# Kernel tuning notes

Measured on AMD Instinct MI355X. Metric: run time of the kernel, lower is better.

The kernel has to match this reference:

```python
import jax, jax.numpy as jnp
import numpy as np

B, C, T = 128, 8, 128   # batch, channels, time steps
K, S = 20, 128          # known classes, barycenter length


def setup_inputs() -> dict:
    key = jax.random.key(0)
    k1, k2, k3, k4, k5 = jax.random.split(key, 5)
    x = jax.random.normal(k1, (B, C, T), dtype=jnp.float32)
    preds = jax.random.randint(k2, (B,), 0, K).astype(jnp.int32)
    barycenters = jax.random.normal(k3, (K, S, C), dtype=jnp.float32)
    # thresholds centered near realistic scales so both detector branches fire
    top_dist = 7.0 + 0.5 * jax.random.normal(k4, (K,), dtype=jnp.float32)
    bottom_cc = 25.0 + 5.0 * jax.random.normal(k5, (K, C), dtype=jnp.float32)
    return {"x": x, "preds": preds, "barycenters": barycenters,
            "top_dist": top_dist, "bottom_cc": bottom_cc}


def _dtw_dist(cost):
    """Classic DTW DP over a [T, S] sq-euclidean cost matrix; returns accumulated cost."""
    inf = jnp.asarray(jnp.inf, cost.dtype)
    row0 = jnp.cumsum(cost[0])  # first row: only left moves

    def row_step(prev, crow):
        prev_shift = jnp.concatenate([jnp.full((1,), inf, cost.dtype), prev[:-1]])
        def col_step(left, inp):
            c, p, ps = inp
            v = c + jnp.minimum(jnp.minimum(p, ps), left)
            return v, v
        _, row = jax.lax.scan(col_step, inf, (crow, prev, prev_shift))
        return row, None

    last, _ = jax.lax.scan(row_step, row0, cost[1:])
    return last[-1]


def reference(x, preds, barycenters, top_dist, bottom_cc):
    xt = jnp.transpose(x, (0, 2, 1))                    # [B, T, C]
    x2 = jnp.sum(xt * xt, axis=-1)                      # [B, T]
    b2 = jnp.sum(barycenters * barycenters, axis=-1)    # [K, S]
    dots = jnp.einsum('btc,ksc->bkts', xt, barycenters)  # [B, K, T, S]
    cost = jnp.maximum(x2[:, None, :, None] + b2[None, :, None, :] - 2.0 * dots, 0.0)

    Bn, Kn, Tn, Sn = cost.shape
    dists = jax.vmap(_dtw_dist)(cost.reshape(Bn * Kn, Tn, Sn)).reshape(Bn, Kn)
    log_dists = jnp.log(dists)
    dtw_unknown = jnp.all(log_dists > top_dist[None, :], axis=1)   # [B]

    # per-channel full cross-correlation max vs each barycenter
    corr_max = lambda a, v: jnp.max(jnp.correlate(a, v, mode='full'))
    per_ch = jax.vmap(corr_max, in_axes=(1, 1))          # over channels -> [C]
    per_cls = jax.vmap(per_ch, in_axes=(None, 0))        # over classes  -> [K, C]
    per_b = jax.vmap(per_cls, in_axes=(0, None))         # over batch    -> [B, K, C]
    ccs = per_b(xt, barycenters)
    # class 'fails' if any channel cc is not above its bottom threshold
    cc_unknown = jnp.all(jnp.any(ccs <= bottom_cc[None, :, :], axis=2), axis=1)  # [B]

    unknown = cc_unknown | dtw_unknown
    return jnp.where(unknown, Kn, preds)
```

## Files before the change

### kernel.cpp

```cpp
#include <hip/hip_runtime.h>
#include <hip/hip_bf16.h>
#include <math.h>

#define B_ 128
#define C_ 8
#define T_ 128
#define K_ 20
#define S_ 128

#define XROW 388
#define BTROW 132
#define SWZ(j) ((j) ^ ((((j) >> 5) & 7) << 2))
#define XP_GUARD 16
#define BT_BASE (4 * XROW + XP_GUARD)
#define SMEMF 3680

template <int CTRL, int RMASK>
__device__ __forceinline__ float dppf(float oldv, float v) {
    return __int_as_float(__builtin_amdgcn_update_dpp(
        __float_as_int(oldv), __float_as_int(v), CTRL, RMASK, 0xf, false));
}

__global__ __launch_bounds__(256) void fused_kernel(const float* __restrict__ x,
                                                    const float* __restrict__ bary,
                                                    const float* __restrict__ top_dist,
                                                    const float* __restrict__ bottom_cc,
                                                    int* __restrict__ dtw_gt,
                                                    int* __restrict__ cc_fail2) {
    __shared__ __align__(16) float smem[SMEMF];
    const float INF = __builtin_inff();
    int u = blockIdx.x;
    int tid = threadIdx.x;
    int w = tid >> 6;
    int lane = tid & 63;

    if (u % 3 == 0) {
        int pg = u / 3;
        int b  = pg / 5;
        int kg = pg - b * 5;
        int kk = kg * 4 + w;
        float* tile = smem;

        {
            int c  = tid >> 5;
            int t0 = (tid & 31) * 4;
            float4 v = *(const float4*)(x + ((size_t)b * C_ + c) * T_ + t0);
            tile[(t0 + 0) * 12 + c] = v.x;
            tile[(t0 + 1) * 12 + c] = v.y;
            tile[(t0 + 2) * 12 + c] = v.z;
            tile[(t0 + 3) * 12 + c] = v.w;
        }
        __syncthreads();
        if (tid < T_) {
            const float* rp = tile + tid * 12;
            float4 xa = *(const float4*)rp;
            float4 xh = *(const float4*)(rp + 4);
            float s = xa.x * xa.x;
            s = fmaf(xa.y, xa.y, s); s = fmaf(xa.z, xa.z, s); s = fmaf(xa.w, xa.w, s);
            s = fmaf(xh.x, xh.x, s); s = fmaf(xh.y, xh.y, s); s = fmaf(xh.z, xh.z, s);
            s = fmaf(xh.w, xh.w, s);
            tile[tid * 12 + 8] = s;
        }
        __syncthreads();

        float bv0[8], bv1[8], B20, B21;
        {
            const float4* bp = (const float4*)(bary + ((size_t)kk * S_ + 2 * lane) * C_);
            float4 q0 = bp[0], q1 = bp[1], q2 = bp[2], q3 = bp[3];
            bv0[0]=q0.x; bv0[1]=q0.y; bv0[2]=q0.z; bv0[3]=q0.w;
            bv0[4]=q1.x; bv0[5]=q1.y; bv0[6]=q1.z; bv0[7]=q1.w;
            bv1[0]=q2.x; bv1[1]=q2.y; bv1[2]=q2.z; bv1[3]=q2.w;
            bv1[4]=q3.x; bv1[5]=q3.y; bv1[6]=q3.z; bv1[7]=q3.w;
            float s0 = 0.f, s1 = 0.f;
            #pragma unroll
            for (int ch = 0; ch < 8; ++ch) {
                s0 = fmaf(bv0[ch], bv0[ch], s0);
                s1 = fmaf(bv1[ch], bv1[ch], s1);
            }
            B20 = s0; B21 = s1;
            #pragma unroll
            for (int ch = 0; ch < 8; ++ch) { bv0[ch] *= -2.f; bv1[ch] *= -2.f; }
        }

        float n0 = INF, n1 = INF;
        float dfix = (lane == 0) ? 0.f : INF;

        __builtin_amdgcn_s_setprio(1);
        float4 xa_n = *(const float4*)tile;
        float4 xh_n = *(const float4*)(tile + 4);
        float x2_n  = tile[8];

        #pragma unroll 2
        for (int t = 0; t < T_; ++t) {
            float4 xa = xa_n, xh = xh_n;
            float X2t = x2_n;
            const float* rpn = tile + ((t + 1) & (T_ - 1)) * 12;
            xa_n = *(const float4*)rpn;
            xh_n = *(const float4*)(rpn + 4);
            x2_n = rpn[8];

            float xv[8];
            xv[0]=xa.x; xv[1]=xa.y; xv[2]=xa.z; xv[3]=xa.w;
            xv[4]=xh.x; xv[5]=xh.y; xv[6]=xh.z; xv[7]=xh.w;
            float a0 = X2t + B20, a1 = X2t + B21;
            #pragma unroll
            for (int ch = 0; ch < 8; ++ch) {
                a0 = fmaf(bv0[ch], xv[ch], a0);
                a1 = fmaf(bv1[ch], xv[ch], a1);
            }
            a0 = fmaxf(a0, 0.f);
            a1 = fmaxf(a1, 0.f);

            float diag = dppf<0x138, 0xf>(INF, n1);
            float m0 = fminf(fminf(n0, diag), dfix);
            float m1 = fminf(n1, n0);
            dfix = INF;
            float C0 = a0 + m0;
            float C1 = a1 + m1;
            float C  = fminf(C1, C0 + a1);
            float A  = a0 + a1;

            float Ci, Ai;
            Ci = dppf<0x111, 0xf>(INF, C); Ai = dppf<0x111, 0xf>(0.f, A);
            C = fminf(C, Ci + A); A = A + Ai;
            Ci = dppf<0x112, 0xf>(INF, C); Ai = dppf<0x112, 0xf>(0.f, A);
            C = fminf(C, Ci + A); A = A + Ai;
            Ci = dppf<0x114, 0xf>(INF, C); Ai = dppf<0x114, 0xf>(0.f, A);
            C = fminf(C, Ci + A); A = A + Ai;
            Ci = dppf<0x118, 0xf>(INF, C); Ai = dppf<0x118, 0xf>(0.f, A);
            C = fminf(C, Ci + A); A = A + Ai;
            Ci = dppf<0x142, 0xa>(INF, C); Ai = dppf<0x142, 0xa>(0.f, A);
            C = fminf(C, Ci + A); A = A + Ai;
            Ci = dppf<0x143, 0xc>(INF, C); Ai = dppf<0x143, 0xc>(0.f, A);
            C = fminf(C, Ci + A); A = A + Ai;

            float Cp = dppf<0x138, 0xf>(INF, C);
            n0 = fminf(C0, Cp + a0);
            n1 = C;
        }
        __builtin_amdgcn_s_setprio(0);

        if (lane == 63)
            dtw_gt[b * K_ + kk] = (logf(n1) > top_dist[kk]) ? 1 : 0;
    } else {
        int cb = u - u / 3 - 1;
        int bh = cb / 5;
        int g5 = cb - bh * 5;
        int b  = bh >> 1;
        int h  = bh & 1;
        int kk = g5 * 4 + w;
        int cbase = h * 4;

        float* xp = smem;
        float* bt = smem + BT_BASE + w * (4 * BTROW);

        const float* xsrc = x + ((size_t)b * C_ + cbase) * T_;
        #pragma unroll
        for (int c = 0; c < 4; ++c) {
            for (int j = tid; j < XROW; j += 256) {
                int t = j - (S_ - 1);
                float v = (t >= 0 && t < T_) ? xsrc[c * T_ + t] : 0.f;
                xp[c * XROW + SWZ(j)] = v;
            }
        }
        #pragma unroll
        for (int r = 0; r < 2; ++r) {
            int s = r * 64 + lane;
            float4 q = *(const float4*)(bary + ((size_t)kk * S_ + s) * C_ + cbase);
            bt[0 * BTROW + s] = q.x;
            bt[1 * BTROW + s] = q.y;
            bt[2 * BTROW + s] = q.z;
            bt[3 * BTROW + s] = q.w;
        }
        __syncthreads();

        int cl = lane >> 4;
        int gl = lane & 15;
        int lag0 = gl << 4;
        const float* xr = xp + cl * XROW;
        const float* br = bt + cl * BTROW;

        float wdw[20];
        #pragma unroll
        for (int i = 0; i < 5; ++i) {
            float4 v = *(const float4*)&xr[SWZ(lag0 + i * 4)];
            wdw[i * 4 + 0] = v.x; wdw[i * 4 + 1] = v.y;
            wdw[i * 4 + 2] = v.z; wdw[i * 4 + 3] = v.w;
        }
        float acc[16];
        #pragma unroll
        for (int j = 0; j < 16; ++j) acc[j] = 0.f;

        #pragma unroll 8
        for (int s4 = 0; s4 < S_; s4 += 4) {
            float4 bq = *(const float4*)&br[s4];
            float bvals[4] = {bq.x, bq.y, bq.z, bq.w};
            #pragma unroll
            for (int uu = 0; uu < 4; ++uu) {
                #pragma unroll
                for (int j = 0; j < 16; ++j)
                    acc[j] = fmaf(wdw[uu + j], bvals[uu], acc[j]);
            }
            #pragma unroll
            for (int i = 0; i < 16; ++i) wdw[i] = wdw[i + 4];
            float4 v = *(const float4*)&xr[SWZ(lag0 + s4 + 20)];
            wdw[16] = v.x; wdw[17] = v.y; wdw[18] = v.z; wdw[19] = v.w;
        }

        if (gl == 15) acc[15] = -INF;
        float m = acc[0];
        #pragma unroll
        for (int j = 1; j < 16; ++j) m = fmaxf(m, acc[j]);
        #pragma unroll
        for (int off = 8; off >= 1; off >>= 1)
            m = fmaxf(m, __shfl_xor(m, off));

        bool fail = false;
        if (gl == 0) fail = (m <= bottom_cc[kk * C_ + cbase + cl]);
        unsigned long long bal = __ballot(fail);
        if (lane == 0) cc_fail2[(b * K_ + kk) * 2 + h] = (bal != 0ULL) ? 1 : 0;
    }
}

__global__ void final_kernel(const int* __restrict__ preds,
                             const int* __restrict__ dtw_gt,
                             const int* __restrict__ cc_fail2,
                             int* __restrict__ out) {
    int b = threadIdx.x;
    if (b < B_) {
        int dtw_all = 1, cc_all = 1;
        #pragma unroll
        for (int k = 0; k < K_; ++k) {
            dtw_all &= dtw_gt[b * K_ + k];
            cc_all &= (cc_fail2[(b * K_ + k) * 2] | cc_fail2[(b * K_ + k) * 2 + 1]);
        }
        out[b] = (dtw_all | cc_all) ? K_ : preds[b];
    }
}

extern "C" void kernel_launch(void* const* d_in, const int* in_sizes, int n_in,
                              void* d_out, int out_size, void* d_ws, size_t ws_size,
                              hipStream_t stream) {
    const float* x         = (const float*)d_in[0];
    const int*   preds     = (const int*)d_in[1];
    const float* bary      = (const float*)d_in[2];
    const float* top_dist  = (const float*)d_in[3];
    const float* bottom_cc = (const float*)d_in[4];
    int* out = (int*)d_out;

    int* dtw_gt   = (int*)d_ws;
    int* cc_fail2 = dtw_gt + B_ * K_;

    fused_kernel<<<1920, 256, 0, stream>>>(x, bary, top_dist, bottom_cc, dtw_gt, cc_fail2);
    final_kernel<<<1, 128, 0, stream>>>(preds, dtw_gt, cc_fail2, out);
}
```

Baseline: 72.43 us.

## Process two DTW class pairs per wave to interleave independent dependency chains

Each DTW wave now computes two (batch,class) DTW recurrences at once, so one block covers 8 pairs instead of 4. The DTW blocks are remapped to every fifth block, which lets a block span two batch rows, so two x tiles are loaded. The grid shrinks from 1920 to 1600 blocks. Interleaving the two independent DPP scan chains is meant to hide the latency of the serial cross-lane scan, at the cost of higher register pressure and fewer DTW waves running in parallel.

```diff
diff --git a/kernel.cpp b/kernel.cpp
--- a/kernel.cpp
+++ b/kernel.cpp
@@ -13,6 +13,7 @@
 #define SWZ(j) ((j) ^ ((((j) >> 5) & 7) << 2))
 #define XP_GUARD 16
 #define BT_BASE (4 * XROW + XP_GUARD)
+#define TILEF 1536
 #define SMEMF 3680
 
 template <int CTRL, int RMASK>
@@ -34,55 +35,78 @@
     int w = tid >> 6;
     int lane = tid & 63;
 
-    if (u % 3 == 0) {
-        int pg = u / 3;
-        int b  = pg / 5;
-        int kg = pg - b * 5;
-        int kk = kg * 4 + w;
-        float* tile = smem;
+    if (u % 5 == 0) {
+        int j  = u / 5;
+        int p0 = j * 8 + w * 2;
+        int b  = p0 / K_;
+        int k0 = p0 - b * K_;
+        int b_lo = (j * 8) / K_;
+        int b_hi = (j * 8 + 7) / K_;
+        float* tile0 = smem;
+        float* tile1 = smem + TILEF;
 
         {
             int c  = tid >> 5;
             int t0 = (tid & 31) * 4;
-            float4 v = *(const float4*)(x + ((size_t)b * C_ + c) * T_ + t0);
-            tile[(t0 + 0) * 12 + c] = v.x;
-            tile[(t0 + 1) * 12 + c] = v.y;
-            tile[(t0 + 2) * 12 + c] = v.z;
-            tile[(t0 + 3) * 12 + c] = v.w;
+            float4 v0 = *(const float4*)(x + ((size_t)b_lo * C_ + c) * T_ + t0);
+            float4 v1 = *(const float4*)(x + ((size_t)b_hi * C_ + c) * T_ + t0);
+            tile0[(t0 + 0) * 12 + c] = v0.x;
+            tile0[(t0 + 1) * 12 + c] = v0.y;
+            tile0[(t0 + 2) * 12 + c] = v0.z;
+            tile0[(t0 + 3) * 12 + c] = v0.w;
+            tile1[(t0 + 0) * 12 + c] = v1.x;
+            tile1[(t0 + 1) * 12 + c] = v1.y;
+            tile1[(t0 + 2) * 12 + c] = v1.z;
+            tile1[(t0 + 3) * 12 + c] = v1.w;
         }
         __syncthreads();
-        if (tid < T_) {
-            const float* rp = tile + tid * 12;
+        {
+            float* tt = (tid < T_) ? tile0 : tile1;
+            int t = tid & (T_ - 1);
+            const float* rp = tt + t * 12;
             float4 xa = *(const float4*)rp;
             float4 xh = *(const float4*)(rp + 4);
             float s = xa.x * xa.x;
             s = fmaf(xa.y, xa.y, s); s = fmaf(xa.z, xa.z, s); s = fmaf(xa.w, xa.w, s);
             s = fmaf(xh.x, xh.x, s); s = fmaf(xh.y, xh.y, s); s = fmaf(xh.z, xh.z, s);
             s = fmaf(xh.w, xh.w, s);
-            tile[tid * 12 + 8] = s;
+            tt[t * 12 + 8] = s;
         }
         __syncthreads();
 
-        float bv0[8], bv1[8], B20, B21;
+        const float* tile = (b == b_lo) ? tile0 : tile1;
+
+        float bvA0[8], bvA1[8], bvB0[8], bvB1[8], B2A0, B2A1, B2B0, B2B1;
         {
-            const float4* bp = (const float4*)(bary + ((size_t)kk * S_ + 2 * lane) * C_);
-            float4 q0 = bp[0], q1 = bp[1], q2 = bp[2], q3 = bp[3];
-            bv0[0]=q0.x; bv0[1]=q0.y; bv0[2]=q0.z; bv0[3]=q0.w;
-            bv0[4]=q1.x; bv0[5]=q1.y; bv0[6]=q1.z; bv0[7]=q1.w;
-            bv1[0]=q2.x; bv1[1]=q2.y; bv1[2]=q2.z; bv1[3]=q2.w;
-            bv1[4]=q3.x; bv1[5]=q3.y; bv1[6]=q3.z; bv1[7]=q3.w;
-            float s0 = 0.f, s1 = 0.f;
+            const float4* bpA = (const float4*)(bary + ((size_t)k0 * S_ + 2 * lane) * C_);
+            const float4* bpB = (const float4*)(bary + ((size_t)(k0 + 1) * S_ + 2 * lane) * C_);
+            float4 qa0 = bpA[0], qa1 = bpA[1], qa2 = bpA[2], qa3 = bpA[3];
+            float4 qb0 = bpB[0], qb1 = bpB[1], qb2 = bpB[2], qb3 = bpB[3];
+            bvA0[0]=qa0.x; bvA0[1]=qa0.y; bvA0[2]=qa0.z; bvA0[3]=qa0.w;
+            bvA0[4]=qa1.x; bvA0[5]=qa1.y; bvA0[6]=qa1.z; bvA0[7]=qa1.w;
+            bvA1[0]=qa2.x; bvA1[1]=qa2.y; bvA1[2]=qa2.z; bvA1[3]=qa2.w;
+            bvA1[4]=qa3.x; bvA1[5]=qa3.y; bvA1[6]=qa3.z; bvA1[7]=qa3.w;
+            bvB0[0]=qb0.x; bvB0[1]=qb0.y; bvB0[2]=qb0.z; bvB0[3]=qb0.w;
+            bvB0[4]=qb1.x; bvB0[5]=qb1.y; bvB0[6]=qb1.z; bvB0[7]=qb1.w;
+            bvB1[0]=qb2.x; bvB1[1]=qb2.y; bvB1[2]=qb2.z; bvB1[3]=qb2.w;
+            bvB1[4]=qb3.x; bvB1[5]=qb3.y; bvB1[6]=qb3.z; bvB1[7]=qb3.w;
+            float sA0=0.f, sA1=0.f, sB0=0.f, sB1=0.f;
             #pragma unroll
             for (int ch = 0; ch < 8; ++ch) {
-                s0 = fmaf(bv0[ch], bv0[ch], s0);
-                s1 = fmaf(bv1[ch], bv1[ch], s1);
-            }
-            B20 = s0; B21 = s1;
-            #pragma unroll
-            for (int ch = 0; ch < 8; ++ch) { bv0[ch] *= -2.f; bv1[ch] *= -2.f; }
-        }
-
-        float n0 = INF, n1 = INF;
+                sA0 = fmaf(bvA0[ch], bvA0[ch], sA0);
+                sA1 = fmaf(bvA1[ch], bvA1[ch], sA1);
+                sB0 = fmaf(bvB0[ch], bvB0[ch], sB0);
+                sB1 = fmaf(bvB1[ch], bvB1[ch], sB1);
+            }
+            B2A0 = sA0; B2A1 = sA1; B2B0 = sB0; B2B1 = sB1;
+            #pragma unroll
+            for (int ch = 0; ch < 8; ++ch) {
+                bvA0[ch] *= -2.f; bvA1[ch] *= -2.f;
+                bvB0[ch] *= -2.f; bvB1[ch] *= -2.f;
+            }
+        }
+
+        float nA0 = INF, nA1 = INF, nB0 = INF, nB1 = INF;
         float dfix = (lane == 0) ? 0.f : INF;
 
         __builtin_amdgcn_s_setprio(1);
@@ -102,48 +126,57 @@
             float xv[8];
             xv[0]=xa.x; xv[1]=xa.y; xv[2]=xa.z; xv[3]=xa.w;
             xv[4]=xh.x; xv[5]=xh.y; xv[6]=xh.z; xv[7]=xh.w;
-            float a0 = X2t + B20, a1 = X2t + B21;
+            float aA0 = X2t + B2A0, aA1 = X2t + B2A1;
+            float aB0 = X2t + B2B0, aB1 = X2t + B2B1;
             #pragma unroll
             for (int ch = 0; ch < 8; ++ch) {
-                a0 = fmaf(bv0[ch], xv[ch], a0);
-                a1 = fmaf(bv1[ch], xv[ch], a1);
-            }
-            a0 = fmaxf(a0, 0.f);
-            a1 = fmaxf(a1, 0.f);
-
-            float diag = dppf<0x138, 0xf>(INF, n1);
-            float m0 = fminf(fminf(n0, diag), dfix);
-            float m1 = fminf(n1, n0);
+                aA0 = fmaf(bvA0[ch], xv[ch], aA0);
+                aA1 = fmaf(bvA1[ch], xv[ch], aA1);
+                aB0 = fmaf(bvB0[ch], xv[ch], aB0);
+                aB1 = fmaf(bvB1[ch], xv[ch], aB1);
+            }
+            aA0 = fmaxf(aA0, 0.f); aA1 = fmaxf(aA1, 0.f);
+            aB0 = fmaxf(aB0, 0.f); aB1 = fmaxf(aB1, 0.f);
+
+            float diagA = dppf<0x138, 0xf>(INF, nA1);
+            float diagB = dppf<0x138, 0xf>(INF, nB1);
+            float mA0 = fminf(fminf(nA0, diagA), dfix);
+            float mB0 = fminf(fminf(nB0, diagB), dfix);
+            float mA1 = fminf(nA1, nA0);
+            float mB1 = fminf(nB1, nB0);
             dfix = INF;
-            float C0 = a0 + m0;
-            float C1 = a1 + m1;
-            float C  = fminf(C1, C0 + a1);
-            float A  = a0 + a1;
-
-            float Ci, Ai;
-            Ci = dppf<0x111, 0xf>(INF, C); Ai = dppf<0x111, 0xf>(0.f, A);
-            C = fminf(C, Ci + A); A = A + Ai;
-            Ci = dppf<0x112, 0xf>(INF, C); Ai = dppf<0x112, 0xf>(0.f, A);
-            C = fminf(C, Ci + A); A = A + Ai;
-            Ci = dppf<0x114, 0xf>(INF, C); Ai = dppf<0x114, 0xf>(0.f, A);
-            C = fminf(C, Ci + A); A = A + Ai;
-            Ci = dppf<0x118, 0xf>(INF, C); Ai = dppf<0x118, 0xf>(0.f, A);
-            C = fminf(C, Ci + A); A = A + Ai;
-            Ci = dppf<0x142, 0xa>(INF, C); Ai = dppf<0x142, 0xa>(0.f, A);
-            C = fminf(C, Ci + A); A = A + Ai;
-            Ci = dppf<0x143, 0xc>(INF, C); Ai = dppf<0x143, 0xc>(0.f, A);
-            C = fminf(C, Ci + A); A = A + Ai;
-
-            float Cp = dppf<0x138, 0xf>(INF, C);
-            n0 = fminf(C0, Cp + a0);
-            n1 = C;
+            float CA0 = aA0 + mA0, CA1 = aA1 + mA1;
+            float CB0 = aB0 + mB0, CB1 = aB1 + mB1;
+            float CA = fminf(CA1, CA0 + aA1);  float AA = aA0 + aA1;
+            float CB = fminf(CB1, CB0 + aB1);  float AB = aB0 + aB1;
+
+            float CiA, AiA, CiB, AiB;
+            #define SCAN_STEP(CTRL, RMASK)                                          \
+                CiA = dppf<CTRL, RMASK>(INF, CA); AiA = dppf<CTRL, RMASK>(0.f, AA); \
+                CiB = dppf<CTRL, RMASK>(INF, CB); AiB = dppf<CTRL, RMASK>(0.f, AB); \
+                CA = fminf(CA, CiA + AA); AA = AA + AiA;                            \
+                CB = fminf(CB, CiB + AB); AB = AB + AiB;
+            SCAN_STEP(0x111, 0xf)
+            SCAN_STEP(0x112, 0xf)
+            SCAN_STEP(0x114, 0xf)
+            SCAN_STEP(0x118, 0xf)
+            SCAN_STEP(0x142, 0xa)
+            SCAN_STEP(0x143, 0xc)
+            #undef SCAN_STEP
+
+            float CpA = dppf<0x138, 0xf>(INF, CA);
+            float CpB = dppf<0x138, 0xf>(INF, CB);
+            nA0 = fminf(CA0, CpA + aA0);  nA1 = CA;
+            nB0 = fminf(CB0, CpB + aB0);  nB1 = CB;
         }
         __builtin_amdgcn_s_setprio(0);
 
-        if (lane == 63)
-            dtw_gt[b * K_ + kk] = (logf(n1) > top_dist[kk]) ? 1 : 0;
+        if (lane == 63) {
+            dtw_gt[p0]     = (logf(nA1) > top_dist[k0])     ? 1 : 0;
+            dtw_gt[p0 + 1] = (logf(nB1) > top_dist[k0 + 1]) ? 1 : 0;
+        }
     } else {
-        int cb = u - u / 3 - 1;
+        int cb = u - u / 5 - 1;
         int bh = cb / 5;
         int g5 = cb - bh * 5;
         int b  = bh >> 1;
@@ -157,10 +190,10 @@
         const float* xsrc = x + ((size_t)b * C_ + cbase) * T_;
         #pragma unroll
         for (int c = 0; c < 4; ++c) {
-            for (int j = tid; j < XROW; j += 256) {
-                int t = j - (S_ - 1);
+            for (int jj = tid; jj < XROW; jj += 256) {
+                int t = jj - (S_ - 1);
                 float v = (t >= 0 && t < T_) ? xsrc[c * T_ + t] : 0.f;
-                xp[c * XROW + SWZ(j)] = v;
+                xp[c * XROW + SWZ(jj)] = v;
             }
         }
         #pragma unroll
@@ -189,7 +222,7 @@
         }
         float acc[16];
         #pragma unroll
-        for (int j = 0; j < 16; ++j) acc[j] = 0.f;
+        for (int jj = 0; jj < 16; ++jj) acc[jj] = 0.f;
 
         #pragma unroll 8
         for (int s4 = 0; s4 < S_; s4 += 4) {
@@ -198,8 +231,8 @@
             #pragma unroll
             for (int uu = 0; uu < 4; ++uu) {
                 #pragma unroll
-                for (int j = 0; j < 16; ++j)
-                    acc[j] = fmaf(wdw[uu + j], bvals[uu], acc[j]);
+                for (int jj = 0; jj < 16; ++jj)
+                    acc[jj] = fmaf(wdw[uu + jj], bvals[uu], acc[jj]);
             }
             #pragma unroll
             for (int i = 0; i < 16; ++i) wdw[i] = wdw[i + 4];
@@ -210,7 +243,7 @@
         if (gl == 15) acc[15] = -INF;
         float m = acc[0];
         #pragma unroll
-        for (int j = 1; j < 16; ++j) m = fmaxf(m, acc[j]);
+        for (int jj = 1; jj < 16; ++jj) m = fmaxf(m, acc[jj]);
         #pragma unroll
         for (int off = 8; off >= 1; off >>= 1)
             m = fmaxf(m, __shfl_xor(m, off));
@@ -251,6 +284,6 @@
     int* dtw_gt   = (int*)d_ws;
     int* cc_fail2 = dtw_gt + B_ * K_;
 
-    fused_kernel<<<1920, 256, 0, stream>>>(x, bary, top_dist, bottom_cc, dtw_gt, cc_fail2);
+    fused_kernel<<<1600, 256, 0, stream>>>(x, bary, top_dist, bottom_cc, dtw_gt, cc_fail2);
     final_kernel<<<1, 128, 0, stream>>>(preds, dtw_gt, cc_fail2, out);
 }
```

New measurement: 77.78 us. 7.4% more time.
